# Kernel optimization log

Measured on AMD Instinct MI355X. Metric: run time of the kernel, lower is better.

## Reference

```python
import jax, jax.numpy as jnp
import numpy as np

N, B, H, C, NF = 200000, 100, 128, 3, 128


def setup_inputs() -> dict:
    key = jax.random.key(0)
    ks = jax.random.split(key, 12)
    def w(k, shape, s=0.05):
        return jax.random.normal(k, shape, jnp.float32) * s
    return dict(
        node_feat=w(ks[0], (N, NF), 1.0),
        coord=w(ks[1], (N, 3), 1.0),
        virtual_node_feat=w(ks[2], (B, NF, C), 1.0),
        virtual_coord=w(ks[3], (B, 3, C), 1.0),
        data_batch=jnp.sort(jax.random.randint(ks[4], (N,), 0, B)),
        We1=w(ks[5], (2 * NF + 1, H)), be1=jnp.zeros((H,), jnp.float32),
        We2=w(ks[6], (H, H)), be2=jnp.zeros((H,), jnp.float32),
        Wc1=w(ks[7], (H, H)), bc1=jnp.zeros((H,), jnp.float32),
        Wc2=w(ks[8], (H, 1), 0.001),  # xavier gain=0.001 layer, no bias
        Wn1=w(ks[9], (2 * H, H)), bn1=jnp.zeros((H,), jnp.float32),
        Wn2=w(ks[10], (H, H)), bn2=jnp.zeros((H,), jnp.float32),
    )


def _segment_mean(x, idx, num_segments):
    # x: [N, d1, d2] -> [num_segments, d1, d2]; mean over nodes of each graph
    sums = jax.ops.segment_sum(x, idx, num_segments=num_segments)
    counts = jax.ops.segment_sum(jnp.ones((x.shape[0],), x.dtype), idx,
                                 num_segments=num_segments)
    return sums / jnp.maximum(counts, 1.0)[:, None, None]


def reference(node_feat, coord, virtual_node_feat, virtual_coord, data_batch,
              We1, be1, We2, be2, Wc1, bc1, Wc2, Wn1, bn1, Wn2, bn2):
    silu = jax.nn.silu
    n, nf = node_feat.shape
    nb, _, c = virtual_coord.shape

    # gather: real node -> its graph's virtual nodes
    diff = virtual_coord[data_batch] - coord[:, :, None]            # [N,3,C]
    radial = jnp.linalg.norm(diff, axis=1)                          # [N,C]

    # edge model (work in [N,C,feat] layout to avoid permutes)
    feat_R = jnp.broadcast_to(node_feat[:, None, :], (n, c, nf))    # [N,C,NF]
    feat_V = virtual_node_feat[data_batch].transpose(0, 2, 1)       # [N,C,NF]
    e_in = jnp.concatenate([feat_R, feat_V, radial[:, :, None]], axis=-1)
    m = silu(e_in @ We1 + be1)
    m = silu(m @ We2 + be2)                                         # [N,C,H]

    # coord model: per (node, virtual-channel) scalar weight
    s = silu(m @ Wc1 + bc1) @ Wc2                                   # [N,C,1]
    trans = diff * s[:, :, 0][:, None, :]                           # [N,3,C]
    virtual_coord = virtual_coord + _segment_mean(trans, data_batch, nb)

    # node model on virtual nodes
    agg = _segment_mean(m, data_batch, nb)                          # [B,C,H]
    n_in = jnp.concatenate([virtual_node_feat.transpose(0, 2, 1), agg], axis=-1)
    h = silu(n_in @ Wn1 + bn1) @ Wn2 + bn2                          # [B,C,H]
    virtual_node_feat = virtual_node_feat + h.transpose(0, 2, 1)    # residual

    return virtual_node_feat, virtual_coord
```

## Files before the change

### kernel.cpp

```cpp
#include <hip/hip_runtime.h>
#include <hip/hip_bf16.h>
#include <math.h>

#define NNODES 200000
#define NGRAPH 100
#define HD     128
#define NCH    3
#define BN     64
#define EROWS  (BN*NCH)
#define ESTR   136

typedef short short8 __attribute__((ext_vector_type(8)));
typedef float f32x4  __attribute__((ext_vector_type(4)));
typedef unsigned int u32x2 __attribute__((ext_vector_type(2)));
typedef unsigned int u32x4 __attribute__((ext_vector_type(4)));

#define MFMA_16x16x32(a,b,c) __builtin_amdgcn_mfma_f32_16x16x32_bf16((a),(b),(c),0,0,0)

__device__ __forceinline__ float bf2f(unsigned short u) {
    return __uint_as_float(((unsigned int)u) << 16);
}
__device__ __forceinline__ unsigned short f2bf(float f) {
    return (unsigned short)((__float_as_uint(f) + 0x8000u) >> 16);
}
__device__ __forceinline__ unsigned int pack2bf(float lo, float hi) {
    unsigned int a = __float_as_uint(lo) + 0x8000u;
    unsigned int b = __float_as_uint(hi) + 0x8000u;
    return __builtin_amdgcn_perm(b, a, 0x07060302u);
}
__device__ __forceinline__ short8 as_short8(u32x4 v) {
    union { u32x4 u; short8 s; } x; x.u = v; return x.s;
}
__device__ __forceinline__ float silu_f(float x) {
    return x * __builtin_amdgcn_rcpf(1.0f + __expf(-x));
}

__global__ void prep_kernel(const float* __restrict__ We1,
                            const float* __restrict__ We2,
                            const float* __restrict__ Wc1,
                            const float* __restrict__ be1,
                            const float* __restrict__ be2,
                            const float* __restrict__ bc1,
                            const float* __restrict__ Wc2,
                            const float* __restrict__ vnf,
                            unsigned short* __restrict__ w1r,
                            unsigned short* __restrict__ w2r,
                            unsigned short* __restrict__ wc1r,
                            float* __restrict__ Q,
                            float* __restrict__ wlast,
                            float* __restrict__ be1f,
                            float* __restrict__ be2f,
                            float* __restrict__ bc1f,
                            float* __restrict__ wc2f,
                            float* __restrict__ zacc) {
    int bid = blockIdx.x;
    if (bid < 192) {
        int t = bid * 256 + threadIdx.x;
        int m  = t / 16384;
        int e  = t % 16384;
        int j  = e & 7;
        int l  = (e >> 3) & 63;
        int ks = (e >> 9) & 3;
        int ct = e >> 11;
        int kf  = ks * 32 + (l >> 4) * 8 + j;
        int col = ct * 16 + (l & 15);
        int srck = (m == 0) ? kf : (((kf & 7) << 4) | (kf >> 3));
        const float*    src = (m == 0) ? We1 : ((m == 1) ? We2 : Wc1);
        unsigned short* dst = (m == 0) ? w1r : ((m == 1) ? w2r : wc1r);
        dst[e] = f2bf(src[srck * 128 + col]);
        if (t < 128) {
            wlast[t] = We1[256 * 128 + t];
            be1f[t]  = be1[t];
            be2f[t]  = be2[t];
            bc1f[t]  = bc1[t];
            wc2f[t]  = Wc2[t];
        }
    } else if (bid < 492) {
        int bc = bid - 192;
        int b = bc / NCH, c = bc % NCH;
        int t = threadIdx.x;
        __shared__ float v[128];
        if (t < 128) v[t] = vnf[(b * 128 + t) * 3 + c];
        __syncthreads();
        if (t < 128) {
            float s = 0.0f;
            for (int k = 0; k < 128; ++k)
                s += v[k] * We1[(128 + k) * 128 + t];
            Q[(b * 3 + c) * 128 + t] = s;
        }
    } else {
        int idx = (bid - 492) * 256 + threadIdx.x;
        if (idx < 39400) zacc[idx] = 0.0f;
    }
}

__global__ __launch_bounds__(256, 2) void egcl_main(
    const float* __restrict__ node_feat,
    const float* __restrict__ coord,
    const float* __restrict__ vcoord,
    const int*   __restrict__ batch,
    const unsigned short* __restrict__ w1r,
    const unsigned short* __restrict__ w2r,
    const unsigned short* __restrict__ wc1r,
    const float* __restrict__ Q,
    const float* __restrict__ wlast,
    const float* __restrict__ be1f,
    const float* __restrict__ be2f,
    const float* __restrict__ bc1f,
    const float* __restrict__ wc2f,
    float* __restrict__ aggsum,
    float* __restrict__ transsum,
    float* __restrict__ cnt)
{
    __shared__ __align__(16) unsigned short e_buf[EROWS * ESTR];
    __shared__ unsigned short sbatch[BN];
    __shared__ unsigned short sseg_start[BN + 1];
    __shared__ unsigned short sseg_b[BN];
    __shared__ int snseg;

    const int tid   = threadIdx.x;
    const int wave  = tid >> 6;
    const int lane  = tid & 63;
    const int lrow  = lane & 15;
    const int lkb   = (lane >> 4) * 8;
    const int rq    = (lane >> 4) * 4;
    const int node0 = blockIdx.x * BN;

    if (tid < BN) {
        int n = node0 + tid;
        int b = batch[n];
        sbatch[tid] = (unsigned short)b;
        int prev = (tid > 0) ? batch[n - 1] : -1;
        unsigned long long mask = __ballot(b != prev);
        int ns = __popcll(mask);
        if (b != prev) {
            int idx = __popcll(mask & ((1ull << tid) - 1ull));
            sseg_start[idx] = (unsigned short)tid;
            sseg_b[idx]     = (unsigned short)b;
        }
        if (tid == 0) { sseg_start[ns] = BN; snseg = ns; }
        float cx = coord[n * 3 + 0];
        float cy = coord[n * 3 + 1];
        float cz = coord[n * 3 + 2];
        for (int c = 0; c < 3; ++c) {
            float dx = vcoord[b * 9 + 0 * 3 + c] - cx;
            float dy = vcoord[b * 9 + 1 * 3 + c] - cy;
            float dz = vcoord[b * 9 + 2 * 3 + c] - cz;
            f32x4 pad;
            pad[0] = dx; pad[1] = dy; pad[2] = dz;
            pad[3] = sqrtf(dx * dx + dy * dy + dz * dz);
            *(f32x4*)&e_buf[(c * 64 + tid) * ESTR + 128] = pad;
        }
    }
    __syncthreads();
    const int nseg = snseg;

    f32x4 acc1[8] = {};
    {
        const float* arow = node_feat + (size_t)(node0 + wave * 16 + lrow) * 128;
        for (int ks = 0; ks < 4; ++ks) {
            f32x4 x0 = *(const f32x4*)(arow + ks * 32 + lkb);
            f32x4 x1 = *(const f32x4*)(arow + ks * 32 + lkb + 4);
            u32x4 av;
            av[0] = pack2bf(x0[0], x0[1]);
            av[1] = pack2bf(x0[2], x0[3]);
            av[2] = pack2bf(x1[0], x1[1]);
            av[3] = pack2bf(x1[2], x1[3]);
            short8 af = as_short8(av);
            for (int ct = 0; ct < 8; ++ct) {
                short8 bfg = *(const short8*)(w1r + ((ct * 4 + ks) * 64 + lane) * 8);
                acc1[ct] = MFMA_16x16x32(af, bfg, acc1[ct]);
            }
        }
    }
    {
        float wl[8];
        #pragma unroll
        for (int ct = 0; ct < 8; ++ct)
            wl[ct] = wlast[ct * 16 + lrow];
        if (nseg == 1) {
            const float* qb = Q + (int)sseg_b[0] * (NCH * HD);
            float qv[3][8];
            #pragma unroll
            for (int c = 0; c < 3; ++c)
                #pragma unroll
                for (int ct = 0; ct < 8; ++ct)
                    qv[c][ct] = qb[c * 128 + ct * 16 + lrow] + be1f[ct * 16 + lrow];
            #pragma unroll
            for (int r = 0; r < 4; ++r) {
                int nl = wave * 16 + rq + r;
                #pragma unroll
                for (int c = 0; c < 3; ++c) {
                    int row = c * 64 + nl;
                    float rad = *(const float*)&e_buf[row * ESTR + 134];
                    float v[8];
                    #pragma unroll
                    for (int ct = 0; ct < 8; ++ct)
                        v[ct] = silu_f(acc1[ct][r] + qv[c][ct] + rad * wl[ct]);
                    u32x4 av;
                    av[0] = pack2bf(v[0], v[1]);
                    av[1] = pack2bf(v[2], v[3]);
                    av[2] = pack2bf(v[4], v[5]);
                    av[3] = pack2bf(v[6], v[7]);
                    *(u32x4*)&e_buf[row * ESTR + lrow * 8] = av;
                }
            }
        } else {
            float bb[8];
            #pragma unroll
            for (int ct = 0; ct < 8; ++ct)
                bb[ct] = be1f[ct * 16 + lrow];
            #pragma unroll
            for (int r = 0; r < 4; ++r) {
                int nl = wave * 16 + rq + r;
                int b  = sbatch[nl];
                #pragma unroll
                for (int c = 0; c < 3; ++c) {
                    int row = c * 64 + nl;
                    float rad = *(const float*)&e_buf[row * ESTR + 134];
                    const float* qb = Q + (b * 3 + c) * 128;
                    float v[8];
                    #pragma unroll
                    for (int ct = 0; ct < 8; ++ct)
                        v[ct] = silu_f(acc1[ct][r] + bb[ct] + qb[ct * 16 + lrow]
                                       + rad * wl[ct]);
                    u32x4 av;
                    av[0] = pack2bf(v[0], v[1]);
                    av[1] = pack2bf(v[2], v[3]);
                    av[2] = pack2bf(v[4], v[5]);
                    av[3] = pack2bf(v[6], v[7]);
                    *(u32x4*)&e_buf[row * ESTR + lrow * 8] = av;
                }
            }
        }
    }

    const int bagg = (nseg == 1) ? (int)sseg_b[0] * (NCH * HD) : 0;

    for (int half = 0; half < 2; ++half) {
        f32x4 acc[3][4] = {};
        for (int ks = 0; ks < 4; ++ks) {
            short8 af[3];
            #pragma unroll
            for (int j = 0; j < 3; ++j)
                af[j] = *(const short8*)(&e_buf[(j * 64 + wave * 16 + lrow) * ESTR +
                                                ks * 32 + lkb]);
            #pragma unroll
            for (int c4 = 0; c4 < 4; ++c4) {
                int ct = half * 4 + c4;
                short8 bfg = *(const short8*)(w2r + ((ct * 4 + ks) * 64 + lane) * 8);
                #pragma unroll
                for (int j = 0; j < 3; ++j)
                    acc[j][c4] = MFMA_16x16x32(af[j], bfg, acc[j][c4]);
            }
        }
        float b0 = be2f[(half * 4 + 0) * 16 + lrow];
        float b1 = be2f[(half * 4 + 1) * 16 + lrow];
        float b2 = be2f[(half * 4 + 2) * 16 + lrow];
        float b3 = be2f[(half * 4 + 3) * 16 + lrow];
        #pragma unroll
        for (int j = 0; j < 3; ++j) {
            float ps0 = 0.f, ps1 = 0.f, ps2 = 0.f, ps3 = 0.f;
            #pragma unroll
            for (int r = 0; r < 4; ++r) {
                int row = j * 64 + wave * 16 + rq + r;
                float v0 = silu_f(acc[j][0][r] + b0);
                float v1 = silu_f(acc[j][1][r] + b1);
                float v2 = silu_f(acc[j][2][r] + b2);
                float v3 = silu_f(acc[j][3][r] + b3);
                ps0 += v0; ps1 += v1; ps2 += v2; ps3 += v3;
                u32x2 dv;
                dv[0] = pack2bf(v0, v1);
                dv[1] = pack2bf(v2, v3);
                *(u32x2*)&e_buf[row * ESTR + lrow * 8 + half * 4] = dv;
            }
            if (nseg == 1) {
                ps0 += __shfl_xor(ps0, 16, 64); ps0 += __shfl_xor(ps0, 32, 64);
                ps1 += __shfl_xor(ps1, 16, 64); ps1 += __shfl_xor(ps1, 32, 64);
                ps2 += __shfl_xor(ps2, 16, 64); ps2 += __shfl_xor(ps2, 32, 64);
                ps3 += __shfl_xor(ps3, 16, 64); ps3 += __shfl_xor(ps3, 32, 64);
                if (lane < 16) {
                    atomicAdd(&aggsum[bagg + j * 128 + (half * 4 + 0) * 16 + lane], ps0);
                    atomicAdd(&aggsum[bagg + j * 128 + (half * 4 + 1) * 16 + lane], ps1);
                    atomicAdd(&aggsum[bagg + j * 128 + (half * 4 + 2) * 16 + lane], ps2);
                    atomicAdd(&aggsum[bagg + j * 128 + (half * 4 + 3) * 16 + lane], ps3);
                }
            }
        }
    }

    float p[3][4] = {};
    for (int half = 0; half < 2; ++half) {
        f32x4 acc[3][4] = {};
        for (int ks = 0; ks < 4; ++ks) {
            short8 af[3];
            #pragma unroll
            for (int j = 0; j < 3; ++j)
                af[j] = *(const short8*)(&e_buf[(j * 64 + wave * 16 + lrow) * ESTR +
                                                ks * 32 + lkb]);
            #pragma unroll
            for (int c4 = 0; c4 < 4; ++c4) {
                int ct = half * 4 + c4;
                short8 bfg = *(const short8*)(wc1r + ((ct * 4 + ks) * 64 + lane) * 8);
                #pragma unroll
                for (int j = 0; j < 3; ++j)
                    acc[j][c4] = MFMA_16x16x32(af[j], bfg, acc[j][c4]);
            }
        }
        float b0 = bc1f[(half * 4 + 0) * 16 + lrow];
        float b1 = bc1f[(half * 4 + 1) * 16 + lrow];
        float b2 = bc1f[(half * 4 + 2) * 16 + lrow];
        float b3 = bc1f[(half * 4 + 3) * 16 + lrow];
        float w0 = wc2f[(half * 4 + 0) * 16 + lrow];
        float w1 = wc2f[(half * 4 + 1) * 16 + lrow];
        float w2 = wc2f[(half * 4 + 2) * 16 + lrow];
        float w3 = wc2f[(half * 4 + 3) * 16 + lrow];
        #pragma unroll
        for (int j = 0; j < 3; ++j) {
            #pragma unroll
            for (int r = 0; r < 4; ++r) {
                float s = p[j][r];
                s += silu_f(acc[j][0][r] + b0) * w0;
                s += silu_f(acc[j][1][r] + b1) * w1;
                s += silu_f(acc[j][2][r] + b2) * w2;
                s += silu_f(acc[j][3][r] + b3) * w3;
                p[j][r] = s;
            }
        }
    }
    for (int j = 0; j < 3; ++j) {
        float p0 = p[j][0], p1 = p[j][1], p2 = p[j][2], p3 = p[j][3];
        #pragma unroll
        for (int off = 1; off < 16; off <<= 1) {
            p0 += __shfl_xor(p0, off, 64);
            p1 += __shfl_xor(p1, off, 64);
            p2 += __shfl_xor(p2, off, 64);
            p3 += __shfl_xor(p3, off, 64);
        }
        if (lrow == 0) {
            int rbase = j * 64 + wave * 16 + rq;
            *(float*)&e_buf[(rbase + 0) * ESTR + 134] = p0;
            *(float*)&e_buf[(rbase + 1) * ESTR + 134] = p1;
            *(float*)&e_buf[(rbase + 2) * ESTR + 134] = p2;
            *(float*)&e_buf[(rbase + 3) * ESTR + 134] = p3;
        }
    }
    __syncthreads();

    if (nseg == 1) {
        int b = sseg_b[0];
        if (wave == 0) {
            float t[9];
            #pragma unroll
            for (int c = 0; c < 3; ++c) {
                int row = c * 64 + lane;
                float sv = *(const float*)&e_buf[row * ESTR + 134];
                float dx = *(const float*)&e_buf[row * ESTR + 128];
                float dy = *(const float*)&e_buf[row * ESTR + 130];
                float dz = *(const float*)&e_buf[row * ESTR + 132];
                t[0 * 3 + c] = dx * sv;
                t[1 * 3 + c] = dy * sv;
                t[2 * 3 + c] = dz * sv;
            }
            #pragma unroll
            for (int off = 1; off < 64; off <<= 1)
                #pragma unroll
                for (int k = 0; k < 9; ++k)
                    t[k] += __shfl_xor(t[k], off, 64);
            if (lane < 9)
                atomicAdd(&transsum[b * 9 + lane],
                          __shfl(t[lane], 0, 64));
            if (lane == 0) atomicAdd(&cnt[b], 64.0f);
        }
    } else {
        for (int sg = 0; sg < nseg; ++sg) {
            int s0 = sseg_start[sg], s1 = sseg_start[sg + 1], b = sseg_b[sg];
            for (int idx = tid; idx < NCH * HD; idx += 256) {
                int c = idx >> 7, pcol = idx & 127;
                float sum = 0.f;
                for (int ii = s0; ii < s1; ++ii)
                    sum += bf2f(e_buf[(c * 64 + ii) * ESTR + pcol]);
                int h = ((pcol & 7) << 4) | (pcol >> 3);
                atomicAdd(&aggsum[(b * 3 + c) * 128 + h], sum);
            }
            if (tid < 9) {
                int d = tid / 3, c = tid % 3;
                float sum = 0.f;
                for (int ii = s0; ii < s1; ++ii)
                    sum += (*(const float*)&e_buf[(c * 64 + ii) * ESTR + 128 + 2 * d])
                           * (*(const float*)&e_buf[(c * 64 + ii) * ESTR + 134]);
                atomicAdd(&transsum[b * 9 + d * 3 + c], sum);
            }
            if (tid == 0) atomicAdd(&cnt[b], (float)(s1 - s0));
        }
    }
}

__global__ void finalize_kernel(const float* __restrict__ vnf,
                                const float* __restrict__ vcoord,
                                const float* __restrict__ Wn1,
                                const float* __restrict__ bn1,
                                const float* __restrict__ Wn2,
                                const float* __restrict__ bn2,
                                const float* __restrict__ aggsum,
                                const float* __restrict__ transsum,
                                const float* __restrict__ cnt,
                                float* __restrict__ out) {
    int b = blockIdx.x / NCH;
    int c = blockIdx.x % NCH;
    int j = threadIdx.x;
    __shared__ float nin[256];
    __shared__ float h1[128];
    float count = fmaxf(cnt[b], 1.0f);
    nin[j]       = vnf[(b * 128 + j) * 3 + c];
    nin[128 + j] = aggsum[(b * 3 + c) * 128 + j] / count;
    __syncthreads();
    float x = bn1[j];
    for (int k = 0; k < 256; ++k)
        x += nin[k] * Wn1[k * 128 + j];
    h1[j] = silu_f(x);
    __syncthreads();
    float y = bn2[j];
    for (int k = 0; k < 128; ++k)
        y += h1[k] * Wn2[k * 128 + j];
    out[(b * 128 + j) * 3 + c] = vnf[(b * 128 + j) * 3 + c] + y;
    if (c == 0 && j < 9) {
        out[NGRAPH * 128 * 3 + b * 9 + j] =
            vcoord[b * 9 + j] + transsum[b * 9 + j] / count;
    }
}

extern "C" void kernel_launch(void* const* d_in, const int* in_sizes, int n_in,
                              void* d_out, int out_size, void* d_ws, size_t ws_size,
                              hipStream_t stream) {
    const float* node_feat = (const float*)d_in[0];
    const float* coord     = (const float*)d_in[1];
    const float* vnf       = (const float*)d_in[2];
    const float* vcoord    = (const float*)d_in[3];
    const int*   batch     = (const int*)d_in[4];
    const float* We1 = (const float*)d_in[5];
    const float* be1 = (const float*)d_in[6];
    const float* We2 = (const float*)d_in[7];
    const float* be2 = (const float*)d_in[8];
    const float* Wc1 = (const float*)d_in[9];
    const float* bc1 = (const float*)d_in[10];
    const float* Wc2 = (const float*)d_in[11];
    const float* Wn1 = (const float*)d_in[12];
    const float* bn1 = (const float*)d_in[13];
    const float* Wn2 = (const float*)d_in[14];
    const float* bn2 = (const float*)d_in[15];

    char* ws = (char*)d_ws;
    float*          aggsum   = (float*)(ws + 0);
    float*          transsum = (float*)(ws + 153600);
    float*          cntp     = (float*)(ws + 157200);
    float*          Q        = (float*)(ws + 157600);
    unsigned short* w1r      = (unsigned short*)(ws + 311200);
    unsigned short* w2r      = (unsigned short*)(ws + 343968);
    unsigned short* wc1r     = (unsigned short*)(ws + 376736);
    float*          wlast    = (float*)(ws + 409504);
    float*          be1f     = (float*)(ws + 410016);
    float*          be2f     = (float*)(ws + 410528);
    float*          bc1f     = (float*)(ws + 411040);
    float*          wc2f     = (float*)(ws + 411552);

    prep_kernel<<<192 + NGRAPH * NCH + 154, 256, 0, stream>>>(
        We1, We2, Wc1, be1, be2, bc1, Wc2, vnf,
        w1r, w2r, wc1r, Q, wlast, be1f, be2f, bc1f, wc2f,
        (float*)ws);

    egcl_main<<<NNODES / BN, 256, 0, stream>>>(
        node_feat, coord, vcoord, batch, w1r, w2r, wc1r, Q,
        wlast, be1f, be2f, bc1f, wc2f, aggsum, transsum, cntp);

    finalize_kernel<<<NGRAPH * NCH, 128, 0, stream>>>(
        vnf, vcoord, Wn1, bn1, Wn2, bn2, aggsum, transsum, cntp,
        (float*)d_out);
}
```

Baseline: 311.3 us.

## Process virtual channels sequentially with single-plane LDS buffer to raise occupancy

Restructures the main kernel to loop over the three virtual channels one at a time, keeping one 64-row bf16 activation plane in LDS instead of three and moving pad/coord data and per-edge scalars into separate small buffers. The smaller LDS footprint and per-channel accumulators let launch bounds rise from 2 to 4 blocks per CU, aimed at better latency hiding. In exchange, each weight fragment (W2, Wc1) is reloaded three times per block instead of being shared across channels, and the multi-segment path adds extra block-wide barriers per channel.

```diff
diff --git a/kernel.cpp b/kernel.cpp
--- a/kernel.cpp
+++ b/kernel.cpp
@@ -12,8 +12,10 @@
 
 typedef short short8 __attribute__((ext_vector_type(8)));
 typedef float f32x4  __attribute__((ext_vector_type(4)));
-typedef unsigned int u32x2 __attribute__((ext_vector_type(2)));
 typedef unsigned int u32x4 __attribute__((ext_vector_type(4)));
+typedef short short8_a __attribute__((ext_vector_type(8), __may_alias__));
+typedef unsigned int u32x4_a __attribute__((ext_vector_type(4), __may_alias__));
+typedef float f32x4_a __attribute__((ext_vector_type(4), __may_alias__));
 
 #define MFMA_16x16x32(a,b,c) __builtin_amdgcn_mfma_f32_16x16x32_bf16((a),(b),(c),0,0,0)
 
@@ -94,7 +96,7 @@
     }
 }
 
-__global__ __launch_bounds__(256, 2) void egcl_main(
+__global__ __launch_bounds__(256, 4) void egcl_main(
     const float* __restrict__ node_feat,
     const float* __restrict__ coord,
     const float* __restrict__ vcoord,
@@ -112,7 +114,9 @@
     float* __restrict__ transsum,
     float* __restrict__ cnt)
 {
-    __shared__ __align__(16) unsigned short e_buf[EROWS * ESTR];
+    __shared__ __align__(16) unsigned short e_plane[BN * ESTR];
+    __shared__ __align__(16) float pad_buf[EROWS * 4];
+    __shared__ float s_vals[EROWS];
     __shared__ unsigned short sbatch[BN];
     __shared__ unsigned short sseg_start[BN + 1];
     __shared__ unsigned short sseg_b[BN];
@@ -125,6 +129,7 @@
     const int lkb   = (lane >> 4) * 8;
     const int rq    = (lane >> 4) * 4;
     const int node0 = blockIdx.x * BN;
+    const int myrow = wave * 16 + lrow;
 
     if (tid < BN) {
         int n = node0 + tid;
@@ -149,7 +154,7 @@
             f32x4 pad;
             pad[0] = dx; pad[1] = dy; pad[2] = dz;
             pad[3] = sqrtf(dx * dx + dy * dy + dz * dz);
-            *(f32x4*)&e_buf[(c * 64 + tid) * ESTR + 128] = pad;
+            *(f32x4_a*)&pad_buf[(c * 64 + tid) * 4] = pad;
         }
     }
     __syncthreads();
@@ -157,7 +162,7 @@
 
     f32x4 acc1[8] = {};
     {
-        const float* arow = node_feat + (size_t)(node0 + wave * 16 + lrow) * 128;
+        const float* arow = node_feat + (size_t)(node0 + myrow) * 128;
         for (int ks = 0; ks < 4; ++ks) {
             f32x4 x0 = *(const f32x4*)(arow + ks * 32 + lkb);
             f32x4 x1 = *(const f32x4*)(arow + ks * 32 + lkb + 4);
@@ -173,177 +178,155 @@
             }
         }
     }
-    {
-        float wl[8];
-        #pragma unroll
-        for (int ct = 0; ct < 8; ++ct)
-            wl[ct] = wlast[ct * 16 + lrow];
+
+    const int bagg = (nseg == 1) ? (int)sseg_b[0] * (NCH * HD) : 0;
+    float wl[8], b1v[8];
+    #pragma unroll
+    for (int ct = 0; ct < 8; ++ct) {
+        wl[ct]  = wlast[ct * 16 + lrow];
+        b1v[ct] = be1f[ct * 16 + lrow];
+    }
+
+    for (int c = 0; c < 3; ++c) {
         if (nseg == 1) {
-            const float* qb = Q + (int)sseg_b[0] * (NCH * HD);
-            float qv[3][8];
-            #pragma unroll
-            for (int c = 0; c < 3; ++c)
-                #pragma unroll
-                for (int ct = 0; ct < 8; ++ct)
-                    qv[c][ct] = qb[c * 128 + ct * 16 + lrow] + be1f[ct * 16 + lrow];
+            const float* qb = Q + bagg + c * 128;
+            float qv[8];
+            #pragma unroll
+            for (int ct = 0; ct < 8; ++ct)
+                qv[ct] = qb[ct * 16 + lrow] + b1v[ct];
             #pragma unroll
             for (int r = 0; r < 4; ++r) {
                 int nl = wave * 16 + rq + r;
-                #pragma unroll
-                for (int c = 0; c < 3; ++c) {
-                    int row = c * 64 + nl;
-                    float rad = *(const float*)&e_buf[row * ESTR + 134];
-                    float v[8];
-                    #pragma unroll
-                    for (int ct = 0; ct < 8; ++ct)
-                        v[ct] = silu_f(acc1[ct][r] + qv[c][ct] + rad * wl[ct]);
-                    u32x4 av;
-                    av[0] = pack2bf(v[0], v[1]);
-                    av[1] = pack2bf(v[2], v[3]);
-                    av[2] = pack2bf(v[4], v[5]);
-                    av[3] = pack2bf(v[6], v[7]);
-                    *(u32x4*)&e_buf[row * ESTR + lrow * 8] = av;
-                }
+                float rad = pad_buf[(c * 64 + nl) * 4 + 3];
+                float v[8];
+                #pragma unroll
+                for (int ct = 0; ct < 8; ++ct)
+                    v[ct] = silu_f(acc1[ct][r] + qv[ct] + rad * wl[ct]);
+                u32x4 av;
+                av[0] = pack2bf(v[0], v[1]);
+                av[1] = pack2bf(v[2], v[3]);
+                av[2] = pack2bf(v[4], v[5]);
+                av[3] = pack2bf(v[6], v[7]);
+                *(u32x4_a*)&e_plane[nl * ESTR + lrow * 8] = av;
             }
         } else {
-            float bb[8];
-            #pragma unroll
-            for (int ct = 0; ct < 8; ++ct)
-                bb[ct] = be1f[ct * 16 + lrow];
             #pragma unroll
             for (int r = 0; r < 4; ++r) {
                 int nl = wave * 16 + rq + r;
                 int b  = sbatch[nl];
-                #pragma unroll
-                for (int c = 0; c < 3; ++c) {
-                    int row = c * 64 + nl;
-                    float rad = *(const float*)&e_buf[row * ESTR + 134];
-                    const float* qb = Q + (b * 3 + c) * 128;
-                    float v[8];
+                float rad = pad_buf[(c * 64 + nl) * 4 + 3];
+                const float* qb = Q + (b * 3 + c) * 128;
+                float v[8];
+                #pragma unroll
+                for (int ct = 0; ct < 8; ++ct)
+                    v[ct] = silu_f(acc1[ct][r] + b1v[ct] + qb[ct * 16 + lrow]
+                                   + rad * wl[ct]);
+                u32x4 av;
+                av[0] = pack2bf(v[0], v[1]);
+                av[1] = pack2bf(v[2], v[3]);
+                av[2] = pack2bf(v[4], v[5]);
+                av[3] = pack2bf(v[6], v[7]);
+                *(u32x4_a*)&e_plane[nl * ESTR + lrow * 8] = av;
+            }
+        }
+        asm volatile("" ::: "memory");
+
+        {
+            f32x4 acc2[8] = {};
+            for (int ks = 0; ks < 4; ++ks) {
+                short8 af = *(const short8_a*)&e_plane[myrow * ESTR + ks * 32 + lkb];
+                #pragma unroll
+                for (int ct = 0; ct < 8; ++ct) {
+                    short8 bfg = *(const short8*)(w2r + ((ct * 4 + ks) * 64 + lane) * 8);
+                    acc2[ct] = MFMA_16x16x32(af, bfg, acc2[ct]);
+                }
+            }
+            float psum[8];
+            #pragma unroll
+            for (int ct = 0; ct < 8; ++ct) psum[ct] = 0.0f;
+            #pragma unroll
+            for (int r = 0; r < 4; ++r) {
+                int nl = wave * 16 + rq + r;
+                float v[8];
+                #pragma unroll
+                for (int ct = 0; ct < 8; ++ct) {
+                    v[ct] = silu_f(acc2[ct][r] + be2f[ct * 16 + lrow]);
+                    psum[ct] += v[ct];
+                }
+                u32x4 av;
+                av[0] = pack2bf(v[0], v[1]);
+                av[1] = pack2bf(v[2], v[3]);
+                av[2] = pack2bf(v[4], v[5]);
+                av[3] = pack2bf(v[6], v[7]);
+                *(u32x4_a*)&e_plane[nl * ESTR + lrow * 8] = av;
+            }
+            if (nseg == 1) {
+                #pragma unroll
+                for (int ct = 0; ct < 8; ++ct) {
+                    psum[ct] += __shfl_xor(psum[ct], 16, 64);
+                    psum[ct] += __shfl_xor(psum[ct], 32, 64);
+                }
+                if (lane < 16) {
                     #pragma unroll
                     for (int ct = 0; ct < 8; ++ct)
-                        v[ct] = silu_f(acc1[ct][r] + bb[ct] + qb[ct * 16 + lrow]
-                                       + rad * wl[ct]);
-                    u32x4 av;
-                    av[0] = pack2bf(v[0], v[1]);
-                    av[1] = pack2bf(v[2], v[3]);
-                    av[2] = pack2bf(v[4], v[5]);
-                    av[3] = pack2bf(v[6], v[7]);
-                    *(u32x4*)&e_buf[row * ESTR + lrow * 8] = av;
-                }
-            }
-        }
-    }
-
-    const int bagg = (nseg == 1) ? (int)sseg_b[0] * (NCH * HD) : 0;
-
-    for (int half = 0; half < 2; ++half) {
-        f32x4 acc[3][4] = {};
-        for (int ks = 0; ks < 4; ++ks) {
-            short8 af[3];
-            #pragma unroll
-            for (int j = 0; j < 3; ++j)
-                af[j] = *(const short8*)(&e_buf[(j * 64 + wave * 16 + lrow) * ESTR +
-                                                ks * 32 + lkb]);
-            #pragma unroll
-            for (int c4 = 0; c4 < 4; ++c4) {
-                int ct = half * 4 + c4;
-                short8 bfg = *(const short8*)(w2r + ((ct * 4 + ks) * 64 + lane) * 8);
-                #pragma unroll
-                for (int j = 0; j < 3; ++j)
-                    acc[j][c4] = MFMA_16x16x32(af[j], bfg, acc[j][c4]);
-            }
-        }
-        float b0 = be2f[(half * 4 + 0) * 16 + lrow];
-        float b1 = be2f[(half * 4 + 1) * 16 + lrow];
-        float b2 = be2f[(half * 4 + 2) * 16 + lrow];
-        float b3 = be2f[(half * 4 + 3) * 16 + lrow];
-        #pragma unroll
-        for (int j = 0; j < 3; ++j) {
-            float ps0 = 0.f, ps1 = 0.f, ps2 = 0.f, ps3 = 0.f;
-            #pragma unroll
-            for (int r = 0; r < 4; ++r) {
-                int row = j * 64 + wave * 16 + rq + r;
-                float v0 = silu_f(acc[j][0][r] + b0);
-                float v1 = silu_f(acc[j][1][r] + b1);
-                float v2 = silu_f(acc[j][2][r] + b2);
-                float v3 = silu_f(acc[j][3][r] + b3);
-                ps0 += v0; ps1 += v1; ps2 += v2; ps3 += v3;
-                u32x2 dv;
-                dv[0] = pack2bf(v0, v1);
-                dv[1] = pack2bf(v2, v3);
-                *(u32x2*)&e_buf[row * ESTR + lrow * 8 + half * 4] = dv;
-            }
-            if (nseg == 1) {
-                ps0 += __shfl_xor(ps0, 16, 64); ps0 += __shfl_xor(ps0, 32, 64);
-                ps1 += __shfl_xor(ps1, 16, 64); ps1 += __shfl_xor(ps1, 32, 64);
-                ps2 += __shfl_xor(ps2, 16, 64); ps2 += __shfl_xor(ps2, 32, 64);
-                ps3 += __shfl_xor(ps3, 16, 64); ps3 += __shfl_xor(ps3, 32, 64);
-                if (lane < 16) {
-                    atomicAdd(&aggsum[bagg + j * 128 + (half * 4 + 0) * 16 + lane], ps0);
-                    atomicAdd(&aggsum[bagg + j * 128 + (half * 4 + 1) * 16 + lane], ps1);
-                    atomicAdd(&aggsum[bagg + j * 128 + (half * 4 + 2) * 16 + lane], ps2);
-                    atomicAdd(&aggsum[bagg + j * 128 + (half * 4 + 3) * 16 + lane], ps3);
-                }
-            }
-        }
-    }
-
-    float p[3][4] = {};
-    for (int half = 0; half < 2; ++half) {
-        f32x4 acc[3][4] = {};
-        for (int ks = 0; ks < 4; ++ks) {
-            short8 af[3];
-            #pragma unroll
-            for (int j = 0; j < 3; ++j)
-                af[j] = *(const short8*)(&e_buf[(j * 64 + wave * 16 + lrow) * ESTR +
-                                                ks * 32 + lkb]);
-            #pragma unroll
-            for (int c4 = 0; c4 < 4; ++c4) {
-                int ct = half * 4 + c4;
-                short8 bfg = *(const short8*)(wc1r + ((ct * 4 + ks) * 64 + lane) * 8);
-                #pragma unroll
-                for (int j = 0; j < 3; ++j)
-                    acc[j][c4] = MFMA_16x16x32(af[j], bfg, acc[j][c4]);
-            }
-        }
-        float b0 = bc1f[(half * 4 + 0) * 16 + lrow];
-        float b1 = bc1f[(half * 4 + 1) * 16 + lrow];
-        float b2 = bc1f[(half * 4 + 2) * 16 + lrow];
-        float b3 = bc1f[(half * 4 + 3) * 16 + lrow];
-        float w0 = wc2f[(half * 4 + 0) * 16 + lrow];
-        float w1 = wc2f[(half * 4 + 1) * 16 + lrow];
-        float w2 = wc2f[(half * 4 + 2) * 16 + lrow];
-        float w3 = wc2f[(half * 4 + 3) * 16 + lrow];
-        #pragma unroll
-        for (int j = 0; j < 3; ++j) {
-            #pragma unroll
-            for (int r = 0; r < 4; ++r) {
-                float s = p[j][r];
-                s += silu_f(acc[j][0][r] + b0) * w0;
-                s += silu_f(acc[j][1][r] + b1) * w1;
-                s += silu_f(acc[j][2][r] + b2) * w2;
-                s += silu_f(acc[j][3][r] + b3) * w3;
-                p[j][r] = s;
-            }
-        }
-    }
-    for (int j = 0; j < 3; ++j) {
-        float p0 = p[j][0], p1 = p[j][1], p2 = p[j][2], p3 = p[j][3];
-        #pragma unroll
-        for (int off = 1; off < 16; off <<= 1) {
-            p0 += __shfl_xor(p0, off, 64);
-            p1 += __shfl_xor(p1, off, 64);
-            p2 += __shfl_xor(p2, off, 64);
-            p3 += __shfl_xor(p3, off, 64);
-        }
-        if (lrow == 0) {
-            int rbase = j * 64 + wave * 16 + rq;
-            *(float*)&e_buf[(rbase + 0) * ESTR + 134] = p0;
-            *(float*)&e_buf[(rbase + 1) * ESTR + 134] = p1;
-            *(float*)&e_buf[(rbase + 2) * ESTR + 134] = p2;
-            *(float*)&e_buf[(rbase + 3) * ESTR + 134] = p3;
-        }
+                        atomicAdd(&aggsum[bagg + c * 128 + ct * 16 + lane], psum[ct]);
+                }
+            }
+        }
+        asm volatile("" ::: "memory");
+
+        {
+            f32x4 acc3[8] = {};
+            for (int ks = 0; ks < 4; ++ks) {
+                short8 af = *(const short8_a*)&e_plane[myrow * ESTR + ks * 32 + lkb];
+                #pragma unroll
+                for (int ct = 0; ct < 8; ++ct) {
+                    short8 bfg = *(const short8*)(wc1r + ((ct * 4 + ks) * 64 + lane) * 8);
+                    acc3[ct] = MFMA_16x16x32(af, bfg, acc3[ct]);
+                }
+            }
+            float p0 = 0.f, p1 = 0.f, p2 = 0.f, p3 = 0.f;
+            #pragma unroll
+            for (int ct = 0; ct < 8; ++ct) {
+                float bb = bc1f[ct * 16 + lrow];
+                float w2 = wc2f[ct * 16 + lrow];
+                p0 += silu_f(acc3[ct][0] + bb) * w2;
+                p1 += silu_f(acc3[ct][1] + bb) * w2;
+                p2 += silu_f(acc3[ct][2] + bb) * w2;
+                p3 += silu_f(acc3[ct][3] + bb) * w2;
+            }
+            #pragma unroll
+            for (int off = 1; off < 16; off <<= 1) {
+                p0 += __shfl_xor(p0, off, 64);
+                p1 += __shfl_xor(p1, off, 64);
+                p2 += __shfl_xor(p2, off, 64);
+                p3 += __shfl_xor(p3, off, 64);
+            }
+            if (lrow == 0) {
+                int rbase = c * 64 + wave * 16 + rq;
+                s_vals[rbase + 0] = p0;
+                s_vals[rbase + 1] = p1;
+                s_vals[rbase + 2] = p2;
+                s_vals[rbase + 3] = p3;
+            }
+        }
+
+        if (nseg > 1) {
+            __syncthreads();
+            for (int sg = 0; sg < nseg; ++sg) {
+                int s0 = sseg_start[sg], s1 = sseg_start[sg + 1], b = sseg_b[sg];
+                if (tid < 128) {
+                    int pcol = tid;
+                    float sum = 0.f;
+                    for (int ii = s0; ii < s1; ++ii)
+                        sum += bf2f(e_plane[ii * ESTR + pcol]);
+                    int h = ((pcol & 7) << 4) | (pcol >> 3);
+                    atomicAdd(&aggsum[(b * 3 + c) * 128 + h], sum);
+                }
+            }
+            __syncthreads();
+        }
+        asm volatile("" ::: "memory");
     }
     __syncthreads();
 
@@ -353,14 +336,11 @@
             float t[9];
             #pragma unroll
             for (int c = 0; c < 3; ++c) {
-                int row = c * 64 + lane;
-                float sv = *(const float*)&e_buf[row * ESTR + 134];
-                float dx = *(const float*)&e_buf[row * ESTR + 128];
-                float dy = *(const float*)&e_buf[row * ESTR + 130];
-                float dz = *(const float*)&e_buf[row * ESTR + 132];
-                t[0 * 3 + c] = dx * sv;
-                t[1 * 3 + c] = dy * sv;
-                t[2 * 3 + c] = dz * sv;
+                f32x4 pd = *(const f32x4_a*)&pad_buf[(c * 64 + lane) * 4];
+                float sv = s_vals[c * 64 + lane];
+                t[0 * 3 + c] = pd[0] * sv;
+                t[1 * 3 + c] = pd[1] * sv;
+                t[2 * 3 + c] = pd[2] * sv;
             }
             #pragma unroll
             for (int off = 1; off < 64; off <<= 1)
@@ -373,25 +353,20 @@
             if (lane == 0) atomicAdd(&cnt[b], 64.0f);
         }
     } else {
-        for (int sg = 0; sg < nseg; ++sg) {
-            int s0 = sseg_start[sg], s1 = sseg_start[sg + 1], b = sseg_b[sg];
-            for (int idx = tid; idx < NCH * HD; idx += 256) {
-                int c = idx >> 7, pcol = idx & 127;
+        if (tid < 9) {
+            int d = tid / 3, c = tid % 3;
+            for (int sg = 0; sg < nseg; ++sg) {
+                int s0 = sseg_start[sg], s1 = sseg_start[sg + 1], b = sseg_b[sg];
                 float sum = 0.f;
                 for (int ii = s0; ii < s1; ++ii)
-                    sum += bf2f(e_buf[(c * 64 + ii) * ESTR + pcol]);
-                int h = ((pcol & 7) << 4) | (pcol >> 3);
-                atomicAdd(&aggsum[(b * 3 + c) * 128 + h], sum);
-            }
-            if (tid < 9) {
-                int d = tid / 3, c = tid % 3;
-                float sum = 0.f;
-                for (int ii = s0; ii < s1; ++ii)
-                    sum += (*(const float*)&e_buf[(c * 64 + ii) * ESTR + 128 + 2 * d])
-                           * (*(const float*)&e_buf[(c * 64 + ii) * ESTR + 134]);
+                    sum += pad_buf[(c * 64 + ii) * 4 + d] * s_vals[c * 64 + ii];
                 atomicAdd(&transsum[b * 9 + d * 3 + c], sum);
             }
-            if (tid == 0) atomicAdd(&cnt[b], (float)(s1 - s0));
+        }
+        if (tid == 0) {
+            for (int sg = 0; sg < nseg; ++sg)
+                atomicAdd(&cnt[sseg_b[sg]],
+                          (float)(sseg_start[sg + 1] - sseg_start[sg]));
         }
     }
 }
```

Measured after the change: 644.5 us. +107.0%, slower.
